# Performance work log

Hardware: AMD Instinct MI355X
Metric: run time of the kernel (lower is better)

## Reference

```python
import jax, jax.numpy as jnp
import numpy as np

K_SIGN = 100000.0   # tanh sharpness approximating sign()
EPS = 1e-05         # acos clamp epsilon


def setup_inputs() -> dict:
    key = jax.random.key(0)
    B, N, KV = 2, 8, 64
    contour = jax.random.uniform(key, (B, N, KV, 2), dtype=jnp.float32)  # values in [0,1]
    return {"contour": contour, "size": 128}


def reference(contour, size):
    b, n, kv, _ = contour.shape
    dt = contour.dtype
    # pixel grid, normalized by size (matches torch meshgrid 'ij' + reshape(-1,2)/size)
    g = jnp.arange(size, dtype=dt)
    mesh = jnp.stack(jnp.meshgrid(g, g, indexing="ij"), axis=-1).reshape(-1, 2) / size  # (S2, 2)

    c = contour.reshape(b * n, 1, kv, 2)          # (bn, 1, kv, 2)
    diff = c - mesh[None, :, None, :]             # (bn, S2, kv, 2)
    roll_diff = jnp.roll(diff, -1, axis=2)        # next vertex

    # sign = diff * swap(roll_diff); sign[...,1]-sign[...,0] = d_y*rd_x - d_x*rd_y
    cross = diff[..., 1] * roll_diff[..., 0] - diff[..., 0] * roll_diff[..., 1]
    sign = jnp.tanh(K_SIGN * cross)               # (bn, S2, kv)

    norm_diff = jnp.linalg.norm(diff, axis=3)
    norm_roll = jnp.linalg.norm(roll_diff, axis=3)
    scalar = jnp.sum(diff * roll_diff, axis=3)
    cosang = jnp.clip(scalar / (norm_diff * norm_roll), -1.0 + EPS, 1.0 - EPS)
    angles = jnp.arccos(cosang)                   # (bn, S2, kv)

    sum_angles = jnp.clip(jnp.abs(jnp.sum(sign * angles, axis=2) / (2.0 * jnp.pi)), 0.0, 1.0)
    return sum_angles.reshape(b, n, size, size)
```

## Files before the change

### kernel.cpp

```cpp
#include <hip/hip_runtime.h>
#include <math.h>

#define BLOCK 256
#define SPLIT 4
#define PPT   2
#define MAX_KV_LDS 1024

typedef float v2f __attribute__((ext_vector_type(2)));

__device__ __forceinline__ float rsq1(float x)  { return __builtin_amdgcn_rsqf(x); }
__device__ __forceinline__ float sqrt1(float x) { return __builtin_amdgcn_sqrtf(x); }
__device__ __forceinline__ float rcp1(float x)  { return __builtin_amdgcn_rcpf(x); }

template <typename VP>
__device__ __forceinline__ v2f winding_partial_pk(VP vsrc, int kv, int k0, int k1,
                                                  v2f mx2, v2f my2)
{
    v2f acc = {0.0f, 0.0f};
    if (k0 >= k1) return acc;
    float2 v = vsrc[k0];
    v2f dx2 = v.x - mx2;
    v2f dy2 = v.y - my2;
    v2f nd2 = dx2 * dx2 + dy2 * dy2;

    #pragma unroll 4
    for (int k = k0; k < k1; ++k) {
        int kn = k + 1;
        if (kn == kv) kn = 0;
        float2 vn = vsrc[kn];
        v2f rx2 = vn.x - mx2;
        v2f ry2 = vn.y - my2;
        v2f cross = dy2 * rx2 - dx2 * ry2;
        v2f dot   = dx2 * rx2 + dy2 * ry2;
        v2f nr2   = rx2 * rx2 + ry2 * ry2;
        v2f n2    = nd2 * nr2;
        v2f inv   = { rsq1(n2.x), rsq1(n2.y) };
        v2f c     = dot * inv;
        c.x = __builtin_amdgcn_fmed3f(c.x, -0.99999f, 0.99999f);
        c.y = __builtin_amdgcn_fmed3f(c.y, -0.99999f, 0.99999f);
        v2f y = { fabsf(c.x), fabsf(c.y) };
        v2f p = -0.0187293f * y + 0.0742610f;
        p = p * y + -0.2121144f;
        p = p * y + 1.5707288f;
        v2f s = { sqrt1(1.0f - y.x), sqrt1(1.0f - y.y) };
        v2f a = s * p;
        v2f ar = 3.14159265358979f - a;
        a.x = (c.x >= 0.0f) ? a.x : ar.x;
        a.y = (c.y >= 0.0f) ? a.y : ar.y;
        v2f t = cross * 200000.0f;
        v2f th;
        th.x = fmaf(-2.0f, rcp1(__expf(t.x) + 1.0f), 1.0f);
        th.y = fmaf(-2.0f, rcp1(__expf(t.y) + 1.0f), 1.0f);
        acc = acc + th * a;
        dx2 = rx2; dy2 = ry2; nd2 = nr2;
    }
    return acc;
}

template <typename VP>
__device__ __forceinline__ float winding_partial(VP vsrc, int kv, int k0, int k1,
                                                 float mx, float my)
{
    float acc = 0.0f;
    if (k0 >= k1) return acc;
    float2 v = vsrc[k0];
    float dx = v.x - mx, dy = v.y - my;
    float nd2 = fmaf(dx, dx, dy * dy);
    for (int k = k0; k < k1; ++k) {
        int kn = k + 1;
        if (kn == kv) kn = 0;
        float2 vn = vsrc[kn];
        float rx = vn.x - mx, ry = vn.y - my;
        float cross = dy * rx - dx * ry;
        float dot   = fmaf(dx, rx, dy * ry);
        float nr2   = fmaf(rx, rx, ry * ry);
        float c = dot * rsq1(nd2 * nr2);
        c = __builtin_amdgcn_fmed3f(c, -0.99999f, 0.99999f);
        float yy = fabsf(c);
        float p = fmaf(-0.0187293f, yy, 0.0742610f);
        p = fmaf(p, yy, -0.2121144f);
        p = fmaf(p, yy, 1.5707288f);
        float a = sqrt1(1.0f - yy) * p;
        a = (c >= 0.0f) ? a : (3.14159265358979f - a);
        float th = fmaf(-2.0f, rcp1(__expf(cross * 200000.0f) + 1.0f), 1.0f);
        acc = fmaf(th, a, acc);
        dx = rx; dy = ry; nd2 = nr2;
    }
    return acc;
}

__global__ __launch_bounds__(BLOCK)
void contour_mask_kernel(const float2* __restrict__ contour,
                         const int* __restrict__ size_ptr,
                         float* __restrict__ out,
                         int out_size, int in0_elems)
{
    __shared__ float2 verts[MAX_KV_LDS];

    const int size     = *size_ptr;
    const int S2       = size * size;
    const int bn_total = out_size / S2;
    const int kv       = in0_elems / (bn_total * 2);

    const int tid  = threadIdx.x;
    const int PIX_PER_BLOCK = (BLOCK / SPLIT) * PPT;
    const int base = blockIdx.x * PIX_PER_BLOCK;

    const int bn0 = base / S2;
    const int rem = base - bn0 * S2;
    const bool one_image = (rem + PIX_PER_BLOCK <= S2) &&
                           (base + PIX_PER_BLOCK <= out_size);
    const bool use_lds = (kv <= MAX_KV_LDS) && one_image;

    if (use_lds) {
        for (int i = tid; i < kv; i += BLOCK)
            verts[i] = contour[(size_t)bn0 * kv + i];
    }
    __syncthreads();

    const int seg = tid & (SPLIT - 1);
    const int q   = (kv + SPLIT - 1) / SPLIT;
    const int k0  = min(seg * q, kv);
    const int k1  = min(k0 + q, kv);
    const float inv_size = 1.0f / (float)size;
    const float INV2PI = 0.15915494309189535f;

    if (use_lds) {
        const int pi0 = rem / size;
        const int pj0 = rem - pi0 * size;
        const int t   = (tid / SPLIT) * PPT;

        int pjA = pj0 + t, piA = pi0;
        while (pjA >= size) { pjA -= size; ++piA; }
        int pjB = pjA + 1, piB = piA;
        if (pjB >= size) { pjB = 0; ++piB; }

        v2f mx2 = { piA * inv_size, piB * inv_size };
        v2f my2 = { pjA * inv_size, pjB * inv_size };

        v2f acc = winding_partial_pk(verts, kv, k0, k1, mx2, my2);
        acc.x += __shfl_xor(acc.x, 1, 64);
        acc.y += __shfl_xor(acc.y, 1, 64);
        acc.x += __shfl_xor(acc.x, 2, 64);
        acc.y += __shfl_xor(acc.y, 2, 64);

        if (seg == 0) {
            float2 res;
            res.x = fminf(fabsf(acc.x) * INV2PI, 1.0f);
            res.y = fminf(fabsf(acc.y) * INV2PI, 1.0f);
            *(float2*)(out + base + t) = res;
        }
    } else {
        #pragma unroll
        for (int px = 0; px < PPT; ++px) {
            const int pixel = base + (tid / SPLIT) * PPT + px;
            float a = 0.0f;
            int bn = 0;
            if (pixel < out_size) {
                bn = pixel / S2;
                const int p  = pixel - bn * S2;
                const int pi = p / size;
                const int pj = p - pi * size;
                a = winding_partial(contour + (size_t)bn * kv, kv, k0, k1,
                                    pi * inv_size, pj * inv_size);
            }
            a += __shfl_xor(a, 1, 64);
            a += __shfl_xor(a, 2, 64);
            if (pixel < out_size && seg == 0)
                out[pixel] = fminf(fabsf(a) * INV2PI, 1.0f);
        }
    }
}

extern "C" void kernel_launch(void* const* d_in, const int* in_sizes, int n_in,
                              void* d_out, int out_size, void* d_ws, size_t ws_size,
                              hipStream_t stream)
{
    const float2* contour  = (const float2*)d_in[0];
    const int*    size_ptr = (const int*)d_in[1];
    float*        out      = (float*)d_out;

    const int PIX_PER_BLOCK = (BLOCK / SPLIT) * PPT;
    const int blocks = (out_size + PIX_PER_BLOCK - 1) / PIX_PER_BLOCK;
    contour_mask_kernel<<<blocks, BLOCK, 0, stream>>>(
        contour, size_ptr, out, out_size, in_sizes[0]);
}
```

Baseline: 68.02 us.

## Replace acos-of-normalized-dot with atan2 polynomial and rational tanh

Recasts each edge's angle as atan2(|cross|, dot), using a min/max reciprocal and an odd polynomial. This removes the norm products, rsqrt, sqrt and clamp. The exp-based tanh becomes a clamped Padé rational approximation, and a wrap-around vertex is appended in LDS so the inner loop needs no modulo check. Each edge now costs fewer transcendental ops, at the price of different approximation error characteristics. Near-zero cross/dot handling and the Padé accuracy may differ from the reference.

```diff
diff --git a/kernel.cpp b/kernel.cpp
--- a/kernel.cpp
+++ b/kernel.cpp
@@ -8,83 +8,76 @@
 
 typedef float v2f __attribute__((ext_vector_type(2)));
 
-__device__ __forceinline__ float rsq1(float x)  { return __builtin_amdgcn_rsqf(x); }
-__device__ __forceinline__ float sqrt1(float x) { return __builtin_amdgcn_sqrtf(x); }
-__device__ __forceinline__ float rcp1(float x)  { return __builtin_amdgcn_rcpf(x); }
+__device__ __forceinline__ float rcp1(float x) { return __builtin_amdgcn_rcpf(x); }
 
-template <typename VP>
-__device__ __forceinline__ v2f winding_partial_pk(VP vsrc, int kv, int k0, int k1,
-                                                  v2f mx2, v2f my2)
+__device__ __forceinline__ v2f edge_term(v2f cross, v2f dot)
+{
+    v2f t = cross * 100000.0f;
+    v2f s = t * t;
+    v2f pn = (s + 105.0f) * s + 945.0f;
+    v2f num = t * pn;
+    v2f qd = (15.0f * s + 420.0f) * s + 945.0f;
+    v2f th;
+    th.x = __builtin_amdgcn_fmed3f(num.x * rcp1(qd.x), -1.0f, 1.0f);
+    th.y = __builtin_amdgcn_fmed3f(num.y * rcp1(qd.y), -1.0f, 1.0f);
+
+    v2f ac = { fabsf(cross.x), fabsf(cross.y) };
+    v2f ad = { fabsf(dot.x),   fabsf(dot.y)   };
+    v2f mn = { fminf(ac.x, ad.x), fminf(ac.y, ad.y) };
+    v2f mx = { fmaxf(ac.x, ad.x), fmaxf(ac.y, ad.y) };
+    v2f a  = { mn.x * rcp1(mx.x), mn.y * rcp1(mx.y) };
+    v2f s2 = a * a;
+    v2f r = 0.0208351f * s2 - 0.0851330f;
+    r = r * s2 + 0.1801410f;
+    r = r * s2 - 0.3302995f;
+    r = r * s2 + 0.9998660f;
+    r = r * a;
+    v2f rhi = 1.57079632679f - r;
+    r.x = (ac.x > ad.x) ? rhi.x : r.x;
+    r.y = (ac.y > ad.y) ? rhi.y : r.y;
+    v2f rneg = 3.14159265359f - r;
+    r.x = (dot.x < 0.0f) ? rneg.x : r.x;
+    r.y = (dot.y < 0.0f) ? rneg.y : r.y;
+
+    return th * r;
+}
+
+__device__ __forceinline__ v2f winding_pk(const float2* __restrict__ verts,
+                                          int k0, int k1, v2f mx2, v2f my2)
 {
     v2f acc = {0.0f, 0.0f};
     if (k0 >= k1) return acc;
-    float2 v = vsrc[k0];
-    v2f dx2 = v.x - mx2;
-    v2f dy2 = v.y - my2;
-    v2f nd2 = dx2 * dx2 + dy2 * dy2;
+    float2 v = verts[k0];
+    v2f dx = v.x - mx2, dy = v.y - my2;
 
     #pragma unroll 4
     for (int k = k0; k < k1; ++k) {
-        int kn = k + 1;
-        if (kn == kv) kn = 0;
-        float2 vn = vsrc[kn];
-        v2f rx2 = vn.x - mx2;
-        v2f ry2 = vn.y - my2;
-        v2f cross = dy2 * rx2 - dx2 * ry2;
-        v2f dot   = dx2 * rx2 + dy2 * ry2;
-        v2f nr2   = rx2 * rx2 + ry2 * ry2;
-        v2f n2    = nd2 * nr2;
-        v2f inv   = { rsq1(n2.x), rsq1(n2.y) };
-        v2f c     = dot * inv;
-        c.x = __builtin_amdgcn_fmed3f(c.x, -0.99999f, 0.99999f);
-        c.y = __builtin_amdgcn_fmed3f(c.y, -0.99999f, 0.99999f);
-        v2f y = { fabsf(c.x), fabsf(c.y) };
-        v2f p = -0.0187293f * y + 0.0742610f;
-        p = p * y + -0.2121144f;
-        p = p * y + 1.5707288f;
-        v2f s = { sqrt1(1.0f - y.x), sqrt1(1.0f - y.y) };
-        v2f a = s * p;
-        v2f ar = 3.14159265358979f - a;
-        a.x = (c.x >= 0.0f) ? a.x : ar.x;
-        a.y = (c.y >= 0.0f) ? a.y : ar.y;
-        v2f t = cross * 200000.0f;
-        v2f th;
-        th.x = fmaf(-2.0f, rcp1(__expf(t.x) + 1.0f), 1.0f);
-        th.y = fmaf(-2.0f, rcp1(__expf(t.y) + 1.0f), 1.0f);
-        acc = acc + th * a;
-        dx2 = rx2; dy2 = ry2; nd2 = nr2;
+        float2 vn = verts[k + 1];
+        v2f rx = vn.x - mx2, ry = vn.y - my2;
+        v2f cross = dy * rx - dx * ry;
+        v2f dot   = dx * rx + dy * ry;
+        acc = acc + edge_term(cross, dot);
+        dx = rx; dy = ry;
     }
     return acc;
 }
 
-template <typename VP>
-__device__ __forceinline__ float winding_partial(VP vsrc, int kv, int k0, int k1,
-                                                 float mx, float my)
+__device__ __forceinline__ float winding_scalar(const float2* __restrict__ vsrc,
+                                                int kv, int k0, int k1,
+                                                float mxs, float mys)
 {
     float acc = 0.0f;
     if (k0 >= k1) return acc;
     float2 v = vsrc[k0];
-    float dx = v.x - mx, dy = v.y - my;
-    float nd2 = fmaf(dx, dx, dy * dy);
+    float dx = v.x - mxs, dy = v.y - mys;
     for (int k = k0; k < k1; ++k) {
-        int kn = k + 1;
-        if (kn == kv) kn = 0;
+        int kn = k + 1; if (kn == kv) kn = 0;
         float2 vn = vsrc[kn];
-        float rx = vn.x - mx, ry = vn.y - my;
-        float cross = dy * rx - dx * ry;
-        float dot   = fmaf(dx, rx, dy * ry);
-        float nr2   = fmaf(rx, rx, ry * ry);
-        float c = dot * rsq1(nd2 * nr2);
-        c = __builtin_amdgcn_fmed3f(c, -0.99999f, 0.99999f);
-        float yy = fabsf(c);
-        float p = fmaf(-0.0187293f, yy, 0.0742610f);
-        p = fmaf(p, yy, -0.2121144f);
-        p = fmaf(p, yy, 1.5707288f);
-        float a = sqrt1(1.0f - yy) * p;
-        a = (c >= 0.0f) ? a : (3.14159265358979f - a);
-        float th = fmaf(-2.0f, rcp1(__expf(cross * 200000.0f) + 1.0f), 1.0f);
-        acc = fmaf(th, a, acc);
-        dx = rx; dy = ry; nd2 = nr2;
+        float rx = vn.x - mxs, ry = vn.y - mys;
+        v2f cross = { dy * rx - dx * ry, 0.0f };
+        v2f dot   = { fmaf(dx, rx, dy * ry), 1.0f };
+        acc += edge_term(cross, dot).x;
+        dx = rx; dy = ry;
     }
     return acc;
 }
@@ -95,7 +88,7 @@
                          float* __restrict__ out,
                          int out_size, int in0_elems)
 {
-    __shared__ float2 verts[MAX_KV_LDS];
+    __shared__ float2 verts[MAX_KV_LDS + 1];
 
     const int size     = *size_ptr;
     const int S2       = size * size;
@@ -115,6 +108,8 @@
     if (use_lds) {
         for (int i = tid; i < kv; i += BLOCK)
             verts[i] = contour[(size_t)bn0 * kv + i];
+        if (tid == 0)
+            verts[kv] = contour[(size_t)bn0 * kv];
     }
     __syncthreads();
 
@@ -138,7 +133,7 @@
         v2f mx2 = { piA * inv_size, piB * inv_size };
         v2f my2 = { pjA * inv_size, pjB * inv_size };
 
-        v2f acc = winding_partial_pk(verts, kv, k0, k1, mx2, my2);
+        v2f acc = winding_pk(verts, k0, k1, mx2, my2);
         acc.x += __shfl_xor(acc.x, 1, 64);
         acc.y += __shfl_xor(acc.y, 1, 64);
         acc.x += __shfl_xor(acc.x, 2, 64);
@@ -155,14 +150,13 @@
         for (int px = 0; px < PPT; ++px) {
             const int pixel = base + (tid / SPLIT) * PPT + px;
             float a = 0.0f;
-            int bn = 0;
             if (pixel < out_size) {
-                bn = pixel / S2;
+                const int bn = pixel / S2;
                 const int p  = pixel - bn * S2;
                 const int pi = p / size;
                 const int pj = p - pi * size;
-                a = winding_partial(contour + (size_t)bn * kv, kv, k0, k1,
-                                    pi * inv_size, pj * inv_size);
+                a = winding_scalar(contour + (size_t)bn * kv, kv, k0, k1,
+                                   pi * inv_size, pj * inv_size);
             }
             a += __shfl_xor(a, 1, 64);
             a += __shfl_xor(a, 2, 64);
```

Measured after the change: 68.41 us. About the same (+0.6%).
